# Kernel tuning notes

Measured on AMD Instinct MI355X. Metric: run time of the kernel, lower is better.

The kernel has to match this reference:

```python
import jax, jax.numpy as jnp
import numpy as np

HEADS = 12
D_MODEL = 768
D_K = D_MODEL // HEADS
BS, SEQ = 2, 4096


def setup_inputs() -> dict:
    key = jax.random.key(0)
    ks = jax.random.split(key, 12)
    s = 1.0 / np.sqrt(D_MODEL)
    return {
        "q": jax.random.normal(ks[0], (BS, SEQ, D_MODEL), jnp.float32),
        "k": jax.random.normal(ks[1], (BS, SEQ, D_MODEL), jnp.float32),
        "v": jax.random.normal(ks[2], (BS, SEQ, D_MODEL), jnp.float32),
        "Wq": jax.random.normal(ks[3], (D_MODEL, D_MODEL), jnp.float32) * s,
        "bq": jax.random.normal(ks[4], (D_MODEL,), jnp.float32) * s,
        "Wk": jax.random.normal(ks[5], (D_MODEL, D_MODEL), jnp.float32) * s,
        "bk": jax.random.normal(ks[6], (D_MODEL,), jnp.float32) * s,
        "Wv": jax.random.normal(ks[7], (D_MODEL, D_MODEL), jnp.float32) * s,
        "bv": jax.random.normal(ks[8], (D_MODEL,), jnp.float32) * s,
        "Wo": jax.random.normal(ks[9], (D_MODEL, D_MODEL), jnp.float32) * s,
        "bo": jax.random.normal(ks[10], (D_MODEL,), jnp.float32) * s,
        "mask": jnp.ones((BS, 1, SEQ), jnp.int32),
    }


def reference(q, k, v, Wq, bq, Wk, bk, Wv, bv, Wo, bo, mask):
    bs, sq, _ = q.shape
    # torch Linear: x @ W.T + b; then reshape to (bs, S, h, d_k) and transpose to (bs, h, S, d_k)
    def proj(x, W, b):
        y = x @ W.T + b
        return y.reshape(bs, -1, HEADS, D_K).transpose(0, 2, 1, 3)
    qh, kh, vh = proj(q, Wq, bq), proj(k, Wk, bk), proj(v, Wv, bv)
    scores = jnp.einsum("bhqd,bhkd->bhqk", qh, kh) / np.sqrt(D_K)
    # mask.unsqueeze(1): [bs,1,1,S_kv], masked_fill where mask == 0
    scores = jnp.where(mask[:, None, :, :] == 0, jnp.float32(-1e9), scores)
    attn = jax.nn.softmax(scores, axis=-1)  # dropout = identity (eval mode)
    ctx = jnp.einsum("bhqk,bhkd->bhqd", attn, vh)
    concat = ctx.transpose(0, 2, 1, 3).reshape(bs, sq, D_MODEL)
    return concat @ Wo.T + bo
```

## Files before the change

kernel.cpp:

```cpp
#include <hip/hip_runtime.h>
#include <hip/hip_bf16.h>

typedef __bf16 bf16x8 __attribute__((ext_vector_type(8)));
typedef float f32x4 __attribute__((ext_vector_type(4)));
typedef unsigned short u16;

#define HEADS 12
#define DK 64
#define DM 768
#define SEQL 4096
#define BSZ 2
#define MROWS (BSZ * SEQL)
#define WELEM (DM * DM)
#define NX 6291456
#define WTOT (4 * WELEM)
#define BTOT (4 * 768)

#define QSCALE 0.180336880434245f
#define EXP2F(x) __builtin_amdgcn_exp2f(x)

__device__ __forceinline__ float bf2f(u16 x) {
    unsigned int u = ((unsigned int)x) << 16;
    return __uint_as_float(u);
}
__device__ __forceinline__ u16 f2bf(float f) {
    unsigned int u = __float_as_uint(f);
    u += 0x7fff + ((u >> 16) & 1);
    return (u16)(u >> 16);
}
__device__ __forceinline__ unsigned int cvt_pk(float lo, float hi) {
#if __has_builtin(__builtin_amdgcn_cvt_pk_bf16_f32)
    auto r = __builtin_amdgcn_cvt_pk_bf16_f32(lo, hi);
    unsigned int u;
    __builtin_memcpy(&u, &r, 4);
    return u;
#else
    return (unsigned int)f2bf(lo) | ((unsigned int)f2bf(hi) << 16);
#endif
}

__global__ void detect_dtype(const u16* __restrict__ q, int* __restrict__ flag) {
    __shared__ int cnt;
    if (threadIdx.x == 0) cnt = 0;
    __syncthreads();
    int c = 0;
    for (int i = threadIdx.x; i < 16384; i += 256) {
        u16 x = q[i];
        if (((x >> 7) & 0xFF) == 0xFF) c++;
    }
    if (c) atomicAdd(&cnt, c);
    __syncthreads();
    if (threadIdx.x == 0) *flag = (cnt > 0) ? 1 : 0;
}

__global__ __launch_bounds__(256) void convert_x(
    const void* __restrict__ X0, const void* __restrict__ X1, const void* __restrict__ X2,
    u16* __restrict__ Xc, const int* __restrict__ flag) {
    const int f32m = *flag;
    int i8 = blockIdx.x * 256 + threadIdx.x;
    if (i8 >= 3 * NX / 8) return;
    int w = i8 / (NX / 8);
    int off8 = i8 - w * (NX / 8);
    const void* src = (w == 0) ? X0 : (w == 1) ? X1 : X2;
    u16* dst = Xc + (size_t)w * NX + (size_t)off8 * 8;
    if (f32m) {
        float4 f0 = ((const float4*)src)[off8 * 2];
        float4 f1 = ((const float4*)src)[off8 * 2 + 1];
        uint4 p = {cvt_pk(f0.x, f0.y), cvt_pk(f0.z, f0.w),
                   cvt_pk(f1.x, f1.y), cvt_pk(f1.z, f1.w)};
        *(uint4*)dst = p;
    } else {
        *(uint4*)dst = ((const uint4*)src)[off8];
    }
}

__global__ __launch_bounds__(256) void convert_wb(
    const void* __restrict__ W0, const void* __restrict__ W1,
    const void* __restrict__ W2, const void* __restrict__ W3,
    const void* __restrict__ B0, const void* __restrict__ B1,
    const void* __restrict__ B2, const void* __restrict__ B3,
    u16* __restrict__ Wc, u16* __restrict__ bc, const int* __restrict__ flag) {
    const int f32m = *flag;
    int i4 = blockIdx.x * 256 + threadIdx.x;
    const int n4 = (WTOT + BTOT) / 4;
    if (i4 >= n4) return;
    int base = i4 * 4;
    const void* src;
    u16* dst;
    int off;
    if (base < WTOT) {
        int w = base / WELEM;
        off = base - w * WELEM;
        src = (w == 0) ? W0 : (w == 1) ? W1 : (w == 2) ? W2 : W3;
        dst = Wc + w * WELEM + off;
    } else {
        int bi = base - WTOT;
        int w = bi / 768;
        off = bi - w * 768;
        src = (w == 0) ? B0 : (w == 1) ? B1 : (w == 2) ? B2 : B3;
        dst = bc + w * 768 + off;
    }
    if (f32m) {
        float4 f = *(const float4*)((const float*)src + off);
        uint2 p = {cvt_pk(f.x, f.y), cvt_pk(f.z, f.w)};
        *(uint2*)dst = p;
    } else {
        *(uint2*)dst = *(const uint2*)((const u16*)src + off);
    }
}

typedef __attribute__((address_space(1))) unsigned int glb_u32;
typedef __attribute__((address_space(3))) unsigned int lds_u32;

__device__ __forceinline__ void gld16(const u16* g, u16* l) {
    __builtin_amdgcn_global_load_lds((glb_u32*)g, (lds_u32*)l, 16, 0, 0);
}

template <int NCH>
__device__ __forceinline__ void stage_g(const u16* gbase, u16* lbase, int tid) {
#pragma unroll
    for (int it = 0; it < NCH / 256; ++it) {
        int c = it * 256 + tid;
        int row = c >> 2, p = c & 3;
        int gc = p ^ (row & 3);
        gld16(gbase + (size_t)row * DM + gc * 8, lbase + c * 8);
    }
}

__global__ __launch_bounds__(256) void gemm_qkv3(
    const u16* __restrict__ Xc, const u16* __restrict__ Wc, const u16* __restrict__ bc,
    u16* __restrict__ Yq, u16* __restrict__ Yk, u16* __restrict__ Yv) {
    __shared__ __align__(16) u16 As[2][128 * 32];
    __shared__ __align__(16) u16 Bs[2][128 * 32];

    const int by  = blockIdx.y;
    const int sel = by / 6;
    const int n0  = (by - sel * 6) * 128;
    const int m0  = blockIdx.x * 128;

    const u16* X  = Xc + (size_t)sel * NX;
    const u16* W  = Wc + (size_t)sel * WELEM;
    const u16* Bp = bc + sel * 768;
    u16* Y = sel == 0 ? Yq : (sel == 1 ? Yk : Yv);
    const float oscale = sel == 0 ? QSCALE : 1.0f;

    const int tid = threadIdx.x, lane = tid & 63, wave = tid >> 6;
    const int wr = (wave >> 1) * 64, wc2 = (wave & 1) * 64;
    const int l15 = lane & 15, quad = lane >> 4;
    const int ck = (quad ^ (l15 & 3)) * 8;

    f32x4 acc[4][4] = {};

    stage_g<512>(X + (size_t)m0 * DM, &As[0][0], tid);
    stage_g<512>(W + (size_t)n0 * DM, &Bs[0][0], tid);
    __syncthreads();

    for (int it = 0; it < 24; ++it) {
        const int cur = it & 1, nxt = cur ^ 1;
        if (it < 23) {
            stage_g<512>(X + (size_t)m0 * DM + (it + 1) * 32, &As[nxt][0], tid);
            stage_g<512>(W + (size_t)n0 * DM + (it + 1) * 32, &Bs[nxt][0], tid);
        }
        bf16x8 a[4], b[4];
#pragma unroll
        for (int i = 0; i < 4; ++i)
            a[i] = *(const bf16x8*)&As[cur][(wr + i * 16 + l15) * 32 + ck];
#pragma unroll
        for (int j = 0; j < 4; ++j)
            b[j] = *(const bf16x8*)&Bs[cur][(wc2 + j * 16 + l15) * 32 + ck];
#pragma unroll
        for (int i = 0; i < 4; ++i)
#pragma unroll
            for (int j = 0; j < 4; ++j)
                acc[i][j] = __builtin_amdgcn_mfma_f32_16x16x32_bf16(a[i], b[j], acc[i][j], 0, 0, 0);
        __syncthreads();
    }

#pragma unroll
    for (int j = 0; j < 4; ++j) {
        int o = n0 + wc2 + j * 16 + l15;
        float bv = bf2f(Bp[o]);
        int h = o >> 6, d = o & 63;
#pragma unroll
        for (int i = 0; i < 4; ++i) {
            int row0 = m0 + wr + i * 16 + quad * 4;
            int bb = row0 >> 12, s0 = row0 & (SEQL - 1);
            if (sel < 2) {
#pragma unroll
                for (int r = 0; r < 4; ++r)
                    Y[((bb * HEADS + h) << 18) + ((s0 + r) << 6) + d] =
                        f2bf((acc[i][j][r] + bv) * oscale);
            } else {
                uint2 p = {cvt_pk(acc[i][j][0] + bv, acc[i][j][1] + bv),
                           cvt_pk(acc[i][j][2] + bv, acc[i][j][3] + bv)};
                *(uint2*)&Y[((bb * HEADS + h) << 18) + (d << 12) + s0] = p;
            }
        }
    }
}

__global__ __launch_bounds__(256) void gemm_out3(const u16* __restrict__ X,
                                                 const u16* __restrict__ W,
                                                 const u16* __restrict__ Bp,
                                                 void* __restrict__ Y,
                                                 const int* __restrict__ flag) {
    __shared__ __align__(16) u16 As[2][64 * 32];
    __shared__ __align__(16) u16 Bs[2][128 * 32];

    const int f32mode = *flag;
    const int m0 = blockIdx.x * 64, n0 = blockIdx.y * 128;
    const int tid = threadIdx.x, lane = tid & 63, wave = tid >> 6;
    const int wr = (wave >> 1) * 32, wc2 = (wave & 1) * 64;
    const int l15 = lane & 15, quad = lane >> 4;
    const int ck = (quad ^ (l15 & 3)) * 8;

    f32x4 acc[2][4] = {};

    stage_g<256>(X + (size_t)m0 * DM, &As[0][0], tid);
    stage_g<512>(W + (size_t)n0 * DM, &Bs[0][0], tid);
    __syncthreads();

    for (int it = 0; it < 24; ++it) {
        const int cur = it & 1, nxt = cur ^ 1;
        if (it < 23) {
            stage_g<256>(X + (size_t)m0 * DM + (it + 1) * 32, &As[nxt][0], tid);
            stage_g<512>(W + (size_t)n0 * DM + (it + 1) * 32, &Bs[nxt][0], tid);
        }
        bf16x8 a[2], b[4];
#pragma unroll
        for (int i = 0; i < 2; ++i)
            a[i] = *(const bf16x8*)&As[cur][(wr + i * 16 + l15) * 32 + ck];
#pragma unroll
        for (int j = 0; j < 4; ++j)
            b[j] = *(const bf16x8*)&Bs[cur][(wc2 + j * 16 + l15) * 32 + ck];
#pragma unroll
        for (int i = 0; i < 2; ++i)
#pragma unroll
            for (int j = 0; j < 4; ++j)
                acc[i][j] = __builtin_amdgcn_mfma_f32_16x16x32_bf16(a[i], b[j], acc[i][j], 0, 0, 0);
        __syncthreads();
    }

#pragma unroll
    for (int j = 0; j < 4; ++j) {
        int o = n0 + wc2 + j * 16 + l15;
        float bv = bf2f(Bp[o]);
#pragma unroll
        for (int i = 0; i < 2; ++i)
#pragma unroll
            for (int r = 0; r < 4; ++r) {
                int row = m0 + wr + i * 16 + quad * 4 + r;
                float val = acc[i][j][r] + bv;
                if (f32mode) ((float*)Y)[(size_t)row * DM + o] = val;
                else         ((u16*)Y)[(size_t)row * DM + o] = f2bf(val);
            }
    }
}

__device__ __forceinline__ void stage8_bf16(u16* dst, const u16* src) {
    *(uint4*)dst = *(const uint4*)src;
}
__device__ __forceinline__ void stage16_bf16(u16* dst, const u16* src) {
    *(uint4*)dst = *(const uint4*)src;
    *(uint4*)(dst + 8) = *(const uint4*)(src + 8);
}
__device__ __forceinline__ void stage16_f32pk(u16* dst, const float* src) {
    float4 f0 = ((const float4*)src)[0];
    float4 f1 = ((const float4*)src)[1];
    float4 f2 = ((const float4*)src)[2];
    float4 f3 = ((const float4*)src)[3];
    uint4 lo = {cvt_pk(f0.x, f0.y), cvt_pk(f0.z, f0.w), cvt_pk(f1.x, f1.y), cvt_pk(f1.z, f1.w)};
    uint4 hi = {cvt_pk(f2.x, f2.y), cvt_pk(f2.z, f2.w), cvt_pk(f3.x, f3.y), cvt_pk(f3.z, f3.w)};
    *(uint4*)dst = lo;
    *(uint4*)(dst + 8) = hi;
}

__global__ __launch_bounds__(256) void gemm_qkv_fb(
    const void* __restrict__ Xq, const void* __restrict__ Xk, const void* __restrict__ Xv,
    const u16* __restrict__ Wc, const u16* __restrict__ bc,
    u16* __restrict__ Yq, u16* __restrict__ Yk, u16* __restrict__ Yv,
    const int* __restrict__ flag) {
    __shared__ __align__(16) u16 As[128][40];
    __shared__ __align__(16) u16 Bs[64][40];
    const int f32mode = *flag;
    const int by = blockIdx.y;
    const int sel = by / 12;
    const int n0 = (by - sel * 12) * 64;
    const int m0 = blockIdx.x * 128;
    const void* Xp = sel == 0 ? Xq : (sel == 1 ? Xk : Xv);
    const u16* Wp = Wc + sel * WELEM;
    const u16* Bp = bc + sel * 768;
    u16* Y = sel == 0 ? Yq : (sel == 1 ? Yk : Yv);
    const float oscale = sel == 0 ? QSCALE : 1.0f;
    const int tid = threadIdx.x, lane = tid & 63, wave = tid >> 6;
    const int wr = (wave >> 1) * 64, wc = (wave & 1) * 32;
    const int l15 = lane & 15, quad = lane >> 4;
    const int srA = tid >> 1, scA = (tid & 1) * 16;
    const int srB = tid >> 2, scB = (tid & 3) * 8;
    f32x4 acc[4][2] = {};
    const size_t xoff = (size_t)(m0 + srA) * DM + scA;
    const size_t woff = (size_t)(n0 + srB) * DM + scB;
    for (int kb = 0; kb < DM; kb += 32) {
        if (f32mode) stage16_f32pk(&As[srA][scA], (const float*)Xp + xoff + kb);
        else         stage16_bf16(&As[srA][scA], (const u16*)Xp + xoff + kb);
        stage8_bf16(&Bs[srB][scB], Wp + woff + kb);
        __syncthreads();
        bf16x8 a[4], b[2];
#pragma unroll
        for (int i = 0; i < 4; ++i) a[i] = *(const bf16x8*)&As[wr + i * 16 + l15][quad * 8];
#pragma unroll
        for (int j = 0; j < 2; ++j) b[j] = *(const bf16x8*)&Bs[wc + j * 16 + l15][quad * 8];
#pragma unroll
        for (int i = 0; i < 4; ++i)
#pragma unroll
            for (int j = 0; j < 2; ++j)
                acc[i][j] = __builtin_amdgcn_mfma_f32_16x16x32_bf16(a[i], b[j], acc[i][j], 0, 0, 0);
        __syncthreads();
    }
#pragma unroll
    for (int j = 0; j < 2; ++j) {
        int o = n0 + wc + j * 16 + l15;
        float bv = bf2f(Bp[o]);
#pragma unroll
        for (int i = 0; i < 4; ++i)
#pragma unroll
            for (int r = 0; r < 4; ++r) {
                int row = m0 + wr + i * 16 + quad * 4 + r;
                float val = (acc[i][j][r] + bv) * oscale;
                int bb = row >> 12, s = row & (SEQL - 1);
                int h = o >> 6, d = o & 63;
                if (sel < 2) Y[((bb * HEADS + h) << 18) + (s << 6) + d] = f2bf(val);
                else         Y[((bb * HEADS + h) << 18) + (d << 12) + s] = f2bf(val);
            }
    }
}

__global__ __launch_bounds__(256) void gemm_out_fb(const u16* __restrict__ X,
                                                   const u16* __restrict__ Wp,
                                                   const u16* __restrict__ Bp,
                                                   void* __restrict__ Y,
                                                   const int* __restrict__ flag) {
    __shared__ __align__(16) u16 As[128][40];
    __shared__ __align__(16) u16 Bs[64][40];
    const int f32mode = *flag;
    const int m0 = blockIdx.x * 128, n0 = blockIdx.y * 64;
    const int tid = threadIdx.x, lane = tid & 63, wave = tid >> 6;
    const int wr = (wave >> 1) * 64, wc = (wave & 1) * 32;
    const int l15 = lane & 15, quad = lane >> 4;
    const int srA = tid >> 1, scA = (tid & 1) * 16;
    const int srB = tid >> 2, scB = (tid & 3) * 8;
    f32x4 acc[4][2] = {};
    const size_t xoff = (size_t)(m0 + srA) * DM + scA;
    const size_t woff = (size_t)(n0 + srB) * DM + scB;
    for (int kb = 0; kb < DM; kb += 32) {
        stage16_bf16(&As[srA][scA], X + xoff + kb);
        stage8_bf16(&Bs[srB][scB], Wp + woff + kb);
        __syncthreads();
        bf16x8 a[4], b[2];
#pragma unroll
        for (int i = 0; i < 4; ++i) a[i] = *(const bf16x8*)&As[wr + i * 16 + l15][quad * 8];
#pragma unroll
        for (int j = 0; j < 2; ++j) b[j] = *(const bf16x8*)&Bs[wc + j * 16 + l15][quad * 8];
#pragma unroll
        for (int i = 0; i < 4; ++i)
#pragma unroll
            for (int j = 0; j < 2; ++j)
                acc[i][j] = __builtin_amdgcn_mfma_f32_16x16x32_bf16(a[i], b[j], acc[i][j], 0, 0, 0);
        __syncthreads();
    }
#pragma unroll
    for (int j = 0; j < 2; ++j) {
        int o = n0 + wc + j * 16 + l15;
        float bv = bf2f(Bp[o]);
#pragma unroll
        for (int i = 0; i < 4; ++i)
#pragma unroll
            for (int r = 0; r < 4; ++r) {
                int row = m0 + wr + i * 16 + quad * 4 + r;
                float val = acc[i][j][r] + bv;
                if (f32mode) ((float*)Y)[(size_t)row * DM + o] = val;
                else         ((u16*)Y)[(size_t)row * DM + o] = f2bf(val);
            }
    }
}

__device__ __forceinline__ void stage_tile(const u16* gbase, int rstride,
                                           u16* lbase, int tid) {
#pragma unroll
    for (int it = 0; it < 2; ++it) {
        int c = it * 256 + tid;
        int row = c >> 3, p = c & 7;
        int gc = p ^ (row & 7);
        gld16(gbase + (size_t)row * rstride + gc * 8, lbase + c * 8);
    }
}

__global__ __launch_bounds__(256, 3) void flash_attn(const u16* __restrict__ Q,
                                                     const u16* __restrict__ K,
                                                     const u16* __restrict__ Vt,
                                                     const int* __restrict__ mask,
                                                     u16* __restrict__ ctx) {
    __shared__ __align__(16) u16 Ks[2][64 * 64];
    __shared__ __align__(16) u16 Vs[2][64 * 64];
    __shared__ __align__(16) float Ms[2][64];
    __shared__ __align__(16) u16 Ps[4][32 * 72];

    const int tid  = threadIdx.x;
    const int lane = tid & 63;
    const int wave = tid >> 6;
    const int l15  = lane & 15;
    const int quad = lane >> 4;

    const int bh = blockIdx.y;
    const int b  = bh / HEADS;
    const int h  = bh - b * HEADS;
    const int qb = blockIdx.x * 128 + wave * 32;

    const u16* Qh = Q  + ((size_t)bh << 18);
    const u16* Kh = K  + ((size_t)bh << 18);
    const u16* Vh = Vt + ((size_t)bh << 18);
    const int* maskb = mask + b * SEQL;

    bf16x8 aq[2][2];
#pragma unroll
    for (int s = 0; s < 2; ++s)
#pragma unroll
        for (int c = 0; c < 2; ++c)
            aq[s][c] = *(const bf16x8*)&Qh[(size_t)(qb + s * 16 + l15) * DK + c * 32 + quad * 8];

    const int r7   = l15 & 7;
    const int ck0  = (quad ^ r7) * 8;
    const int ck1  = ((quad + 4) ^ r7) * 8;
    const int lrow = l15 * 64;

    float m_s[2] = {-3.0e38f, -3.0e38f}, l_s[2] = {0.f, 0.f};
    f32x4 o_acc[2][4] = {};

    int mreg = 0;
    if (tid < 64) mreg = maskb[tid];
    stage_tile(Kh, DK, &Ks[0][0], tid);
    stage_tile(Vh, SEQL, &Vs[0][0], tid);
    if (tid < 64) {
        Ms[0][tid] = (mreg == 0) ? -1.0e9f : 0.0f;
        mreg = maskb[64 + tid];
    }
    __syncthreads();

    for (int t = 0; t < 64; ++t) {
        const int cur = t & 1, nxt = cur ^ 1;
        if (t < 63) {
            const int kt = (t + 1) * 64;
            stage_tile(Kh + (size_t)kt * DK, DK, &Ks[nxt][0], tid);
            stage_tile(Vh + kt, SEQL, &Vs[nxt][0], tid);
            if (tid < 64) {
                Ms[nxt][tid] = (mreg == 0) ? -1.0e9f : 0.0f;
                if (t < 62) mreg = maskb[(t + 2) * 64 + tid];
            }
        }

        const u16* kb = &Ks[cur][0];
        const u16* vb = &Vs[cur][0];

        f32x4 s4[2][4];
#pragma unroll
        for (int nt = 0; nt < 4; ++nt) {
            bf16x8 ak0 = *(const bf16x8*)&kb[lrow + nt * 1024 + ck0];
            bf16x8 ak1 = *(const bf16x8*)&kb[lrow + nt * 1024 + ck1];
            f32x4 bias = *(const f32x4*)&Ms[cur][nt * 16 + quad * 4];
#pragma unroll
            for (int s = 0; s < 2; ++s) {
                f32x4 z = {};
                z = __builtin_amdgcn_mfma_f32_16x16x32_bf16(ak0, aq[s][0], z, 0, 0, 0);
                z = __builtin_amdgcn_mfma_f32_16x16x32_bf16(ak1, aq[s][1], z, 0, 0, 0);
#pragma unroll
                for (int r = 0; r < 4; ++r) s4[s][nt][r] = z[r] + bias[r];
            }
        }

        float newm[2], rs[2];
#pragma unroll
        for (int s = 0; s < 2; ++s) {
            float mx = -3.0e38f;
#pragma unroll
            for (int nt = 0; nt < 4; ++nt)
#pragma unroll
                for (int r = 0; r < 4; ++r) mx = fmaxf(mx, s4[s][nt][r]);
            mx = fmaxf(mx, __shfl_xor(mx, 16, 64));
            mx = fmaxf(mx, __shfl_xor(mx, 32, 64));
            newm[s] = fmaxf(m_s[s], mx);

            float r2 = 0.f;
#pragma unroll
            for (int nt = 0; nt < 4; ++nt)
#pragma unroll
                for (int r = 0; r < 4; ++r) {
                    float p = EXP2F(s4[s][nt][r] - newm[s]);
                    s4[s][nt][r] = p;
                    r2 += p;
                }
            r2 += __shfl_xor(r2, 16, 64);
            r2 += __shfl_xor(r2, 32, 64);
            rs[s] = r2;
        }

        if (!__all(newm[0] == m_s[0] && newm[1] == m_s[1])) {
#pragma unroll
            for (int s = 0; s < 2; ++s) {
                float alpha = EXP2F(m_s[s] - newm[s]);
                l_s[s] *= alpha;
#pragma unroll
                for (int dv = 0; dv < 4; ++dv)
#pragma unroll
                    for (int r = 0; r < 4; ++r) o_acc[s][dv][r] *= alpha;
                m_s[s] = newm[s];
            }
        }
        l_s[0] += rs[0];
        l_s[1] += rs[1];

#pragma unroll
        for (int s = 0; s < 2; ++s)
#pragma unroll
            for (int nt = 0; nt < 4; ++nt) {
                uint2 cv = {cvt_pk(s4[s][nt][0], s4[s][nt][1]),
                            cvt_pk(s4[s][nt][2], s4[s][nt][3])};
                *(uint2*)&Ps[wave][(s * 16 + l15) * 72 + nt * 16 + quad * 4] = cv;
            }
        asm volatile("" ::: "memory");

        bf16x8 bp[2][2];
#pragma unroll
        for (int s = 0; s < 2; ++s)
#pragma unroll
            for (int c = 0; c < 2; ++c)
                bp[s][c] = *(const bf16x8*)&Ps[wave][(s * 16 + l15) * 72 + c * 32 + quad * 8];

#pragma unroll
        for (int dv = 0; dv < 4; ++dv) {
            bf16x8 av0 = *(const bf16x8*)&vb[lrow + dv * 1024 + ck0];
            bf16x8 av1 = *(const bf16x8*)&vb[lrow + dv * 1024 + ck1];
#pragma unroll
            for (int s = 0; s < 2; ++s) {
                o_acc[s][dv] = __builtin_amdgcn_mfma_f32_16x16x32_bf16(av0, bp[s][0], o_acc[s][dv], 0, 0, 0);
                o_acc[s][dv] = __builtin_amdgcn_mfma_f32_16x16x32_bf16(av1, bp[s][1], o_acc[s][dv], 0, 0, 0);
            }
        }
        __syncthreads();
    }

#pragma unroll
    for (int s = 0; s < 2; ++s) {
        float inv = 1.0f / l_s[s];
#pragma unroll
        for (int dv = 0; dv < 4; ++dv) {
            uint2 cv = {cvt_pk(o_acc[s][dv][0] * inv, o_acc[s][dv][1] * inv),
                        cvt_pk(o_acc[s][dv][2] * inv, o_acc[s][dv][3] * inv)};
            *(uint2*)&Ps[wave][(s * 16 + l15) * 72 + dv * 16 + quad * 4] = cv;
        }
    }
    asm volatile("" ::: "memory");
    {
        int rowq = lane >> 2, dchunk = lane & 3;
#pragma unroll
        for (int s = 0; s < 2; ++s) {
            uint4 w0 = *(const uint4*)&Ps[wave][(s * 16 + rowq) * 72 + dchunk * 16];
            uint4 w1 = *(const uint4*)&Ps[wave][(s * 16 + rowq) * 72 + dchunk * 16 + 8];
            size_t orow = (size_t)(b * SEQL + qb + s * 16 + rowq) * DM + h * DK + dchunk * 16;
            *(uint4*)&ctx[orow] = w0;
            *(uint4*)&ctx[orow + 8] = w1;
        }
    }
}

extern "C" void kernel_launch(void* const* d_in, const int* in_sizes, int n_in,
                              void* d_out, int out_size, void* d_ws, size_t ws_size,
                              hipStream_t stream) {
    const void* q   = d_in[0];
    const void* k   = d_in[1];
    const void* v   = d_in[2];
    const void* Wq  = d_in[3];
    const void* bq  = d_in[4];
    const void* Wk  = d_in[5];
    const void* bk  = d_in[6];
    const void* Wv  = d_in[7];
    const void* bv  = d_in[8];
    const void* Wo  = d_in[9];
    const void* bo  = d_in[10];
    const int* mask = (const int*)d_in[11];

    const size_t NSH = (size_t)NX;
    u16* ws = (u16*)d_ws;

    const size_t need_full = (6 * NSH + WTOT + BTOT) * sizeof(u16) + 64;
    const size_t need_fb   = (4 * NSH + WTOT + BTOT) * sizeof(u16) + 64;

    if (ws_size >= need_full) {
        u16* Qh  = ws;
        u16* Kh  = ws + NSH;
        u16* Vth = ws + 2 * NSH;
        u16* Xc  = ws + 3 * NSH;
        u16* ctx = Xc;
        u16* Wc  = ws + 6 * NSH;
        u16* bc  = Wc + WTOT;
        int* dflag = (int*)(bc + BTOT);

        detect_dtype<<<1, 256, 0, stream>>>((const u16*)q, dflag);
        convert_x<<<(3 * NX / 8 + 255) / 256, 256, 0, stream>>>(q, k, v, Xc, dflag);
        convert_wb<<<((WTOT + BTOT) / 4 + 255) / 256, 256, 0, stream>>>(
            Wq, Wk, Wv, Wo, bq, bk, bv, bo, Wc, bc, dflag);

        gemm_qkv3<<<dim3(MROWS / 128, 18), 256, 0, stream>>>(Xc, Wc, bc, Qh, Kh, Vth);
        flash_attn<<<dim3(SEQL / 128, BSZ * HEADS), 256, 0, stream>>>(Qh, Kh, Vth, mask, ctx);
        gemm_out3<<<dim3(MROWS / 64, 6), 256, 0, stream>>>(
            ctx, Wc + 3 * (size_t)WELEM, bc + 3 * 768, d_out, dflag);
    } else if (ws_size >= need_fb) {
        u16* Qh  = ws;
        u16* Kh  = ws + NSH;
        u16* Vth = ws + 2 * NSH;
        u16* ctx = ws + 3 * NSH;
        u16* Wc  = ws + 4 * NSH;
        u16* bc  = Wc + WTOT;
        int* dflag = (int*)(bc + BTOT);

        detect_dtype<<<1, 256, 0, stream>>>((const u16*)q, dflag);
        convert_wb<<<((WTOT + BTOT) / 4 + 255) / 256, 256, 0, stream>>>(
            Wq, Wk, Wv, Wo, bq, bk, bv, bo, Wc, bc, dflag);
        gemm_qkv_fb<<<dim3(MROWS / 128, 36), 256, 0, stream>>>(
            q, k, v, Wc, bc, Qh, Kh, Vth, dflag);
        flash_attn<<<dim3(SEQL / 128, BSZ * HEADS), 256, 0, stream>>>(Qh, Kh, Vth, mask, ctx);
        gemm_out_fb<<<dim3(MROWS / 128, 12), 256, 0, stream>>>(
            ctx, Wc + 3 * (size_t)WELEM, bc + 3 * 768, d_out, dflag);
    }
}
```

Before: 416.0 us.

## Restructure flash attention to 8 waves of 16 query rows with register-resident P

Flash attention now launches 512 threads per block, with each of 8 waves owning 16 query rows instead of 4 waves owning 32. The softmax probabilities stay in registers and feed a 16x16x16 bf16 MFMA directly, which removes the per-wave LDS round trip for P. V fragments are read from the swizzled tile in 4-element pieces. The mask bias add is skipped when a tile has no masked keys, and K/V tile staging is spread across twice as many threads. In exchange, each K/V tile is reused by fewer rows per wave, the smaller MFMA shape may have lower throughput, and the extra waves raise occupancy and scheduling pressure.

```diff
diff --git a/kernel.cpp b/kernel.cpp
--- a/kernel.cpp
+++ b/kernel.cpp
@@ -2,6 +2,8 @@
 #include <hip/hip_bf16.h>
 
 typedef __bf16 bf16x8 __attribute__((ext_vector_type(8)));
+typedef __bf16 bf16x4 __attribute__((ext_vector_type(4)));
+typedef short s16x4 __attribute__((ext_vector_type(4)));
 typedef float f32x4 __attribute__((ext_vector_type(4)));
 typedef unsigned short u16;
 
@@ -36,6 +38,21 @@
     return u;
 #else
     return (unsigned int)f2bf(lo) | ((unsigned int)f2bf(hi) << 16);
+#endif
+}
+
+__device__ __forceinline__ f32x4 mfma16(bf16x4 a, bf16x4 b, f32x4 c) {
+#if __has_builtin(__builtin_amdgcn_mfma_f32_16x16x16_bf16)
+    return __builtin_amdgcn_mfma_f32_16x16x16_bf16(a, b, c, 0, 0, 0);
+#elif __has_builtin(__builtin_amdgcn_mfma_f32_16x16x16bf16_1k)
+    s16x4 ai, bi;
+    __builtin_memcpy(&ai, &a, 8);
+    __builtin_memcpy(&bi, &b, 8);
+    return __builtin_amdgcn_mfma_f32_16x16x16bf16_1k(ai, bi, c, 0, 0, 0);
+#else
+    f32x4 d = c;
+    asm("v_mfma_f32_16x16x16_bf16 %0, %1, %2, %0" : "+v"(d) : "v"(a), "v"(b));
+    return d;
 #endif
 }
 
@@ -384,26 +401,21 @@
     }
 }
 
-__device__ __forceinline__ void stage_tile(const u16* gbase, int rstride,
-                                           u16* lbase, int tid) {
-#pragma unroll
-    for (int it = 0; it < 2; ++it) {
-        int c = it * 256 + tid;
-        int row = c >> 3, p = c & 7;
-        int gc = p ^ (row & 7);
-        gld16(gbase + (size_t)row * rstride + gc * 8, lbase + c * 8);
-    }
-}
-
-__global__ __launch_bounds__(256, 3) void flash_attn(const u16* __restrict__ Q,
+__device__ __forceinline__ void stage_tile8(const u16* gbase, int rstride,
+                                            u16* lbase, int tid) {
+    int row = tid >> 3, p = tid & 7;
+    int gc = p ^ (row & 7);
+    gld16(gbase + (size_t)row * rstride + gc * 8, lbase + tid * 8);
+}
+
+__global__ __launch_bounds__(512, 6) void flash_attn(const u16* __restrict__ Q,
                                                      const u16* __restrict__ K,
                                                      const u16* __restrict__ Vt,
                                                      const int* __restrict__ mask,
                                                      u16* __restrict__ ctx) {
-    __shared__ __align__(16) u16 Ks[2][64 * 64];
-    __shared__ __align__(16) u16 Vs[2][64 * 64];
+    __shared__ __align__(16) u16 KVs[2][2][64 * 64];
     __shared__ __align__(16) float Ms[2][64];
-    __shared__ __align__(16) u16 Ps[4][32 * 72];
+    __shared__ int Mf[2];
 
     const int tid  = threadIdx.x;
     const int lane = tid & 63;
@@ -414,34 +426,36 @@
     const int bh = blockIdx.y;
     const int b  = bh / HEADS;
     const int h  = bh - b * HEADS;
-    const int qb = blockIdx.x * 128 + wave * 32;
+    const int qb = blockIdx.x * 128 + wave * 16;
 
     const u16* Qh = Q  + ((size_t)bh << 18);
     const u16* Kh = K  + ((size_t)bh << 18);
     const u16* Vh = Vt + ((size_t)bh << 18);
     const int* maskb = mask + b * SEQL;
 
-    bf16x8 aq[2][2];
-#pragma unroll
-    for (int s = 0; s < 2; ++s)
-#pragma unroll
-        for (int c = 0; c < 2; ++c)
-            aq[s][c] = *(const bf16x8*)&Qh[(size_t)(qb + s * 16 + l15) * DK + c * 32 + quad * 8];
+    bf16x8 aq[2];
+#pragma unroll
+    for (int c = 0; c < 2; ++c)
+        aq[c] = *(const bf16x8*)&Qh[(size_t)(qb + l15) * DK + c * 32 + quad * 8];
 
     const int r7   = l15 & 7;
     const int ck0  = (quad ^ r7) * 8;
     const int ck1  = ((quad + 4) ^ r7) * 8;
     const int lrow = l15 * 64;
-
-    float m_s[2] = {-3.0e38f, -3.0e38f}, l_s[2] = {0.f, 0.f};
-    f32x4 o_acc[2][4] = {};
+    const int vq   = quad >> 1;
+    const int voff = (quad & 1) * 4;
+
+    float m_s = -3.0e38f, l_s = 0.f;
+    f32x4 o_acc[4] = {};
 
     int mreg = 0;
     if (tid < 64) mreg = maskb[tid];
-    stage_tile(Kh, DK, &Ks[0][0], tid);
-    stage_tile(Vh, SEQL, &Vs[0][0], tid);
+    stage_tile8(Kh, DK, &KVs[0][0][0], tid);
+    stage_tile8(Vh, SEQL, &KVs[0][1][0], tid);
     if (tid < 64) {
+        int anym = __any(mreg == 0);
         Ms[0][tid] = (mreg == 0) ? -1.0e9f : 0.0f;
+        if (tid == 0) Mf[0] = anym;
         mreg = maskb[64 + tid];
     }
     __syncthreads();
@@ -450,125 +464,111 @@
         const int cur = t & 1, nxt = cur ^ 1;
         if (t < 63) {
             const int kt = (t + 1) * 64;
-            stage_tile(Kh + (size_t)kt * DK, DK, &Ks[nxt][0], tid);
-            stage_tile(Vh + kt, SEQL, &Vs[nxt][0], tid);
+            stage_tile8(Kh + (size_t)kt * DK, DK, &KVs[nxt][0][0], tid);
+            stage_tile8(Vh + kt, SEQL, &KVs[nxt][1][0], tid);
             if (tid < 64) {
+                int anym = __any(mreg == 0);
                 Ms[nxt][tid] = (mreg == 0) ? -1.0e9f : 0.0f;
+                if (tid == 0) Mf[nxt] = anym;
                 if (t < 62) mreg = maskb[(t + 2) * 64 + tid];
             }
         }
 
-        const u16* kb = &Ks[cur][0];
-        const u16* vb = &Vs[cur][0];
-
-        f32x4 s4[2][4];
+        const u16* kb = &KVs[cur][0][0];
+        const u16* vb = &KVs[cur][1][0];
+        const int usebias = Mf[cur];
+
+        f32x4 s4[4];
 #pragma unroll
         for (int nt = 0; nt < 4; ++nt) {
             bf16x8 ak0 = *(const bf16x8*)&kb[lrow + nt * 1024 + ck0];
             bf16x8 ak1 = *(const bf16x8*)&kb[lrow + nt * 1024 + ck1];
-            f32x4 bias = *(const f32x4*)&Ms[cur][nt * 16 + quad * 4];
-#pragma unroll
-            for (int s = 0; s < 2; ++s) {
-                f32x4 z = {};
-                z = __builtin_amdgcn_mfma_f32_16x16x32_bf16(ak0, aq[s][0], z, 0, 0, 0);
-                z = __builtin_amdgcn_mfma_f32_16x16x32_bf16(ak1, aq[s][1], z, 0, 0, 0);
-#pragma unroll
-                for (int r = 0; r < 4; ++r) s4[s][nt][r] = z[r] + bias[r];
+            f32x4 z = {};
+            z = __builtin_amdgcn_mfma_f32_16x16x32_bf16(ak0, aq[0], z, 0, 0, 0);
+            z = __builtin_amdgcn_mfma_f32_16x16x32_bf16(ak1, aq[1], z, 0, 0, 0);
+            s4[nt] = z;
+        }
+        if (usebias) {
+#pragma unroll
+            for (int nt = 0; nt < 4; ++nt) {
+                f32x4 bias = *(const f32x4*)&Ms[cur][nt * 16 + quad * 4];
+#pragma unroll
+                for (int r = 0; r < 4; ++r) s4[nt][r] += bias[r];
             }
         }
 
-        float newm[2], rs[2];
-#pragma unroll
-        for (int s = 0; s < 2; ++s) {
-            float mx = -3.0e38f;
+        float t0 = fmaxf(fmaxf(s4[0][0], s4[0][1]), fmaxf(s4[0][2], s4[0][3]));
+        float t1 = fmaxf(fmaxf(s4[1][0], s4[1][1]), fmaxf(s4[1][2], s4[1][3]));
+        float t2 = fmaxf(fmaxf(s4[2][0], s4[2][1]), fmaxf(s4[2][2], s4[2][3]));
+        float t3 = fmaxf(fmaxf(s4[3][0], s4[3][1]), fmaxf(s4[3][2], s4[3][3]));
+        float mx = fmaxf(fmaxf(t0, t1), fmaxf(t2, t3));
+        mx = fmaxf(mx, __shfl_xor(mx, 16, 64));
+        mx = fmaxf(mx, __shfl_xor(mx, 32, 64));
+        float newm = fmaxf(m_s, mx);
+
+        f32x4 psum = {};
+#pragma unroll
+        for (int nt = 0; nt < 4; ++nt)
+#pragma unroll
+            for (int r = 0; r < 4; ++r) {
+                float p = EXP2F(s4[nt][r] - newm);
+                s4[nt][r] = p;
+                psum[nt] += p;
+            }
+        float r2 = (psum[0] + psum[1]) + (psum[2] + psum[3]);
+        r2 += __shfl_xor(r2, 16, 64);
+        r2 += __shfl_xor(r2, 32, 64);
+
+        if (!__all(newm == m_s)) {
+            float alpha = EXP2F(m_s - newm);
+            l_s *= alpha;
+#pragma unroll
+            for (int dv = 0; dv < 4; ++dv)
+#pragma unroll
+                for (int r = 0; r < 4; ++r) o_acc[dv][r] *= alpha;
+            m_s = newm;
+        }
+        l_s += r2;
+
+        bf16x4 pp[4];
+#pragma unroll
+        for (int nt = 0; nt < 4; ++nt) {
+            uint2 cv = {cvt_pk(s4[nt][0], s4[nt][1]), cvt_pk(s4[nt][2], s4[nt][3])};
+            __builtin_memcpy(&pp[nt], &cv, 8);
+        }
+
+#pragma unroll
+        for (int dv = 0; dv < 4; ++dv) {
+            bf16x4 av[4];
 #pragma unroll
             for (int nt = 0; nt < 4; ++nt)
-#pragma unroll
-                for (int r = 0; r < 4; ++r) mx = fmaxf(mx, s4[s][nt][r]);
-            mx = fmaxf(mx, __shfl_xor(mx, 16, 64));
-            mx = fmaxf(mx, __shfl_xor(mx, 32, 64));
-            newm[s] = fmaxf(m_s[s], mx);
-
-            float r2 = 0.f;
+                av[nt] = *(const bf16x4*)&vb[(dv * 16 + l15) * 64 +
+                                            (((nt << 1) | vq) ^ r7) * 8 + voff];
 #pragma unroll
             for (int nt = 0; nt < 4; ++nt)
-#pragma unroll
-                for (int r = 0; r < 4; ++r) {
-                    float p = EXP2F(s4[s][nt][r] - newm[s]);
-                    s4[s][nt][r] = p;
-                    r2 += p;
-                }
-            r2 += __shfl_xor(r2, 16, 64);
-            r2 += __shfl_xor(r2, 32, 64);
-            rs[s] = r2;
-        }
-
-        if (!__all(newm[0] == m_s[0] && newm[1] == m_s[1])) {
-#pragma unroll
-            for (int s = 0; s < 2; ++s) {
-                float alpha = EXP2F(m_s[s] - newm[s]);
-                l_s[s] *= alpha;
-#pragma unroll
-                for (int dv = 0; dv < 4; ++dv)
-#pragma unroll
-                    for (int r = 0; r < 4; ++r) o_acc[s][dv][r] *= alpha;
-                m_s[s] = newm[s];
-            }
-        }
-        l_s[0] += rs[0];
-        l_s[1] += rs[1];
-
-#pragma unroll
-        for (int s = 0; s < 2; ++s)
-#pragma unroll
-            for (int nt = 0; nt < 4; ++nt) {
-                uint2 cv = {cvt_pk(s4[s][nt][0], s4[s][nt][1]),
-                            cvt_pk(s4[s][nt][2], s4[s][nt][3])};
-                *(uint2*)&Ps[wave][(s * 16 + l15) * 72 + nt * 16 + quad * 4] = cv;
-            }
-        asm volatile("" ::: "memory");
-
-        bf16x8 bp[2][2];
-#pragma unroll
-        for (int s = 0; s < 2; ++s)
-#pragma unroll
-            for (int c = 0; c < 2; ++c)
-                bp[s][c] = *(const bf16x8*)&Ps[wave][(s * 16 + l15) * 72 + c * 32 + quad * 8];
-
+                o_acc[dv] = mfma16(av[nt], pp[nt], o_acc[dv]);
+        }
+        __syncthreads();
+    }
+
+    u16* eb = &KVs[0][0][0] + wave * 1152;
+    {
+        float inv = 1.0f / l_s;
 #pragma unroll
         for (int dv = 0; dv < 4; ++dv) {
-            bf16x8 av0 = *(const bf16x8*)&vb[lrow + dv * 1024 + ck0];
-            bf16x8 av1 = *(const bf16x8*)&vb[lrow + dv * 1024 + ck1];
-#pragma unroll
-            for (int s = 0; s < 2; ++s) {
-                o_acc[s][dv] = __builtin_amdgcn_mfma_f32_16x16x32_bf16(av0, bp[s][0], o_acc[s][dv], 0, 0, 0);
-                o_acc[s][dv] = __builtin_amdgcn_mfma_f32_16x16x32_bf16(av1, bp[s][1], o_acc[s][dv], 0, 0, 0);
-            }
-        }
-        __syncthreads();
-    }
-
-#pragma unroll
-    for (int s = 0; s < 2; ++s) {
-        float inv = 1.0f / l_s[s];
-#pragma unroll
-        for (int dv = 0; dv < 4; ++dv) {
-            uint2 cv = {cvt_pk(o_acc[s][dv][0] * inv, o_acc[s][dv][1] * inv),
-                        cvt_pk(o_acc[s][dv][2] * inv, o_acc[s][dv][3] * inv)};
-            *(uint2*)&Ps[wave][(s * 16 + l15) * 72 + dv * 16 + quad * 4] = cv;
+            uint2 cv = {cvt_pk(o_acc[dv][0] * inv, o_acc[dv][1] * inv),
+                        cvt_pk(o_acc[dv][2] * inv, o_acc[dv][3] * inv)};
+            *(uint2*)&eb[l15 * 72 + dv * 16 + quad * 4] = cv;
         }
     }
     asm volatile("" ::: "memory");
     {
         int rowq = lane >> 2, dchunk = lane & 3;
-#pragma unroll
-        for (int s = 0; s < 2; ++s) {
-            uint4 w0 = *(const uint4*)&Ps[wave][(s * 16 + rowq) * 72 + dchunk * 16];
-            uint4 w1 = *(const uint4*)&Ps[wave][(s * 16 + rowq) * 72 + dchunk * 16 + 8];
-            size_t orow = (size_t)(b * SEQL + qb + s * 16 + rowq) * DM + h * DK + dchunk * 16;
-            *(uint4*)&ctx[orow] = w0;
-            *(uint4*)&ctx[orow + 8] = w1;
-        }
+        uint4 w0 = *(const uint4*)&eb[rowq * 72 + dchunk * 16];
+        uint4 w1 = *(const uint4*)&eb[rowq * 72 + dchunk * 16 + 8];
+        size_t orow = (size_t)(b * SEQL + qb + rowq) * DM + h * DK + dchunk * 16;
+        *(uint4*)&ctx[orow] = w0;
+        *(uint4*)&ctx[orow + 8] = w1;
     }
 }
 
@@ -610,7 +610,7 @@
             Wq, Wk, Wv, Wo, bq, bk, bv, bo, Wc, bc, dflag);
 
         gemm_qkv3<<<dim3(MROWS / 128, 18), 256, 0, stream>>>(Xc, Wc, bc, Qh, Kh, Vth);
-        flash_attn<<<dim3(SEQL / 128, BSZ * HEADS), 256, 0, stream>>>(Qh, Kh, Vth, mask, ctx);
+        flash_attn<<<dim3(SEQL / 128, BSZ * HEADS), 512, 0, stream>>>(Qh, Kh, Vth, mask, ctx);
         gemm_out3<<<dim3(MROWS / 64, 6), 256, 0, stream>>>(
             ctx, Wc + 3 * (size_t)WELEM, bc + 3 * 768, d_out, dflag);
     } else if (ws_size >= need_fb) {
@@ -627,7 +627,7 @@
             Wq, Wk, Wv, Wo, bq, bk, bv, bo, Wc, bc, dflag);
         gemm_qkv_fb<<<dim3(MROWS / 128, 36), 256, 0, stream>>>(
             q, k, v, Wc, bc, Qh, Kh, Vth, dflag);
-        flash_attn<<<dim3(SEQL / 128, BSZ * HEADS), 256, 0, stream>>>(Qh, Kh, Vth, mask, ctx);
+        flash_attn<<<dim3(SEQL / 128, BSZ * HEADS), 512, 0, stream>>>(Qh, Kh, Vth, mask, ctx);
         gemm_out_fb<<<dim3(MROWS / 128, 12), 256, 0, stream>>>(
             ctx, Wc + 3 * (size_t)WELEM, bc + 3 * 768, d_out, dflag);
     }
```

Result: slower. 472.3 us (+13.5%).

## Feed softmax probabilities to PV MFMA from registers, skip mask bias when unmasked

Applied to the files above, without the earlier changes.

The PV product now uses 16x16x16 MFMAs whose B operand layout matches the S accumulator layout. The bf16 probabilities go straight from registers into the MFMA, removing the per-wave LDS write and read-back of P. The mask bias add is skipped for tiles where a per-tile flag shows no masked keys. The change also adds tree-shaped max and sum reductions and raises wave priority around the MFMA block. The P buffer is gone, which frees LDS for occupancy, and the epilogue reuses the K/V buffers; the cost is twice as many smaller MFMA instructions and narrower V loads.

```diff
diff --git a/kernel.cpp b/kernel.cpp
--- a/kernel.cpp
+++ b/kernel.cpp
@@ -2,6 +2,8 @@
 #include <hip/hip_bf16.h>
 
 typedef __bf16 bf16x8 __attribute__((ext_vector_type(8)));
+typedef __bf16 bf16x4 __attribute__((ext_vector_type(4)));
+typedef short s16x4 __attribute__((ext_vector_type(4)));
 typedef float f32x4 __attribute__((ext_vector_type(4)));
 typedef unsigned short u16;
 
@@ -36,6 +38,21 @@
     return u;
 #else
     return (unsigned int)f2bf(lo) | ((unsigned int)f2bf(hi) << 16);
+#endif
+}
+
+__device__ __forceinline__ f32x4 mfma16(bf16x4 a, bf16x4 b, f32x4 c) {
+#if __has_builtin(__builtin_amdgcn_mfma_f32_16x16x16_bf16)
+    return __builtin_amdgcn_mfma_f32_16x16x16_bf16(a, b, c, 0, 0, 0);
+#elif __has_builtin(__builtin_amdgcn_mfma_f32_16x16x16bf16_1k)
+    s16x4 ai, bi;
+    __builtin_memcpy(&ai, &a, 8);
+    __builtin_memcpy(&bi, &b, 8);
+    return __builtin_amdgcn_mfma_f32_16x16x16bf16_1k(ai, bi, c, 0, 0, 0);
+#else
+    f32x4 d = c;
+    asm("v_mfma_f32_16x16x16_bf16 %0, %1, %2, %0" : "+v"(d) : "v"(a), "v"(b));
+    return d;
 #endif
 }
 
@@ -400,10 +417,9 @@
                                                      const u16* __restrict__ Vt,
                                                      const int* __restrict__ mask,
                                                      u16* __restrict__ ctx) {
-    __shared__ __align__(16) u16 Ks[2][64 * 64];
-    __shared__ __align__(16) u16 Vs[2][64 * 64];
+    __shared__ __align__(16) u16 KVs[2][2][64 * 64];
     __shared__ __align__(16) float Ms[2][64];
-    __shared__ __align__(16) u16 Ps[4][32 * 72];
+    __shared__ int Mf[2];
 
     const int tid  = threadIdx.x;
     const int lane = tid & 63;
@@ -432,16 +448,20 @@
     const int ck0  = (quad ^ r7) * 8;
     const int ck1  = ((quad + 4) ^ r7) * 8;
     const int lrow = l15 * 64;
+    const int vq   = quad >> 1;
+    const int voff = (quad & 1) * 4;
 
     float m_s[2] = {-3.0e38f, -3.0e38f}, l_s[2] = {0.f, 0.f};
     f32x4 o_acc[2][4] = {};
 
     int mreg = 0;
     if (tid < 64) mreg = maskb[tid];
-    stage_tile(Kh, DK, &Ks[0][0], tid);
-    stage_tile(Vh, SEQL, &Vs[0][0], tid);
+    stage_tile(Kh, DK, &KVs[0][0][0], tid);
+    stage_tile(Vh, SEQL, &KVs[0][1][0], tid);
     if (tid < 64) {
+        int anym = __any(mreg == 0);
         Ms[0][tid] = (mreg == 0) ? -1.0e9f : 0.0f;
+        if (tid == 0) Mf[0] = anym;
         mreg = maskb[64 + tid];
     }
     __syncthreads();
@@ -450,54 +470,66 @@
         const int cur = t & 1, nxt = cur ^ 1;
         if (t < 63) {
             const int kt = (t + 1) * 64;
-            stage_tile(Kh + (size_t)kt * DK, DK, &Ks[nxt][0], tid);
-            stage_tile(Vh + kt, SEQL, &Vs[nxt][0], tid);
+            stage_tile(Kh + (size_t)kt * DK, DK, &KVs[nxt][0][0], tid);
+            stage_tile(Vh + kt, SEQL, &KVs[nxt][1][0], tid);
             if (tid < 64) {
+                int anym = __any(mreg == 0);
                 Ms[nxt][tid] = (mreg == 0) ? -1.0e9f : 0.0f;
+                if (tid == 0) Mf[nxt] = anym;
                 if (t < 62) mreg = maskb[(t + 2) * 64 + tid];
             }
         }
 
-        const u16* kb = &Ks[cur][0];
-        const u16* vb = &Vs[cur][0];
+        const u16* kb = &KVs[cur][0][0];
+        const u16* vb = &KVs[cur][1][0];
+        const int usebias = Mf[cur];
 
         f32x4 s4[2][4];
 #pragma unroll
         for (int nt = 0; nt < 4; ++nt) {
             bf16x8 ak0 = *(const bf16x8*)&kb[lrow + nt * 1024 + ck0];
             bf16x8 ak1 = *(const bf16x8*)&kb[lrow + nt * 1024 + ck1];
-            f32x4 bias = *(const f32x4*)&Ms[cur][nt * 16 + quad * 4];
 #pragma unroll
             for (int s = 0; s < 2; ++s) {
                 f32x4 z = {};
                 z = __builtin_amdgcn_mfma_f32_16x16x32_bf16(ak0, aq[s][0], z, 0, 0, 0);
                 z = __builtin_amdgcn_mfma_f32_16x16x32_bf16(ak1, aq[s][1], z, 0, 0, 0);
-#pragma unroll
-                for (int r = 0; r < 4; ++r) s4[s][nt][r] = z[r] + bias[r];
+                s4[s][nt] = z;
+            }
+        }
+        if (usebias) {
+#pragma unroll
+            for (int nt = 0; nt < 4; ++nt) {
+                f32x4 bias = *(const f32x4*)&Ms[cur][nt * 16 + quad * 4];
+#pragma unroll
+                for (int s = 0; s < 2; ++s)
+#pragma unroll
+                    for (int r = 0; r < 4; ++r) s4[s][nt][r] += bias[r];
             }
         }
 
         float newm[2], rs[2];
 #pragma unroll
         for (int s = 0; s < 2; ++s) {
-            float mx = -3.0e38f;
-#pragma unroll
-            for (int nt = 0; nt < 4; ++nt)
-#pragma unroll
-                for (int r = 0; r < 4; ++r) mx = fmaxf(mx, s4[s][nt][r]);
+            float t0 = fmaxf(fmaxf(s4[s][0][0], s4[s][0][1]), fmaxf(s4[s][0][2], s4[s][0][3]));
+            float t1 = fmaxf(fmaxf(s4[s][1][0], s4[s][1][1]), fmaxf(s4[s][1][2], s4[s][1][3]));
+            float t2 = fmaxf(fmaxf(s4[s][2][0], s4[s][2][1]), fmaxf(s4[s][2][2], s4[s][2][3]));
+            float t3 = fmaxf(fmaxf(s4[s][3][0], s4[s][3][1]), fmaxf(s4[s][3][2], s4[s][3][3]));
+            float mx = fmaxf(fmaxf(t0, t1), fmaxf(t2, t3));
             mx = fmaxf(mx, __shfl_xor(mx, 16, 64));
             mx = fmaxf(mx, __shfl_xor(mx, 32, 64));
             newm[s] = fmaxf(m_s[s], mx);
 
-            float r2 = 0.f;
+            f32x4 psum = {};
 #pragma unroll
             for (int nt = 0; nt < 4; ++nt)
 #pragma unroll
                 for (int r = 0; r < 4; ++r) {
                     float p = EXP2F(s4[s][nt][r] - newm[s]);
                     s4[s][nt][r] = p;
-                    r2 += p;
+                    psum[nt] += p;
                 }
+            float r2 = (psum[0] + psum[1]) + (psum[2] + psum[3]);
             r2 += __shfl_xor(r2, 16, 64);
             r2 += __shfl_xor(r2, 32, 64);
             rs[s] = r2;
@@ -518,36 +550,37 @@
         l_s[0] += rs[0];
         l_s[1] += rs[1];
 
+        bf16x4 pp[2][4];
 #pragma unroll
         for (int s = 0; s < 2; ++s)
 #pragma unroll
             for (int nt = 0; nt < 4; ++nt) {
                 uint2 cv = {cvt_pk(s4[s][nt][0], s4[s][nt][1]),
                             cvt_pk(s4[s][nt][2], s4[s][nt][3])};
-                *(uint2*)&Ps[wave][(s * 16 + l15) * 72 + nt * 16 + quad * 4] = cv;
-            }
-        asm volatile("" ::: "memory");
-
-        bf16x8 bp[2][2];
-#pragma unroll
-        for (int s = 0; s < 2; ++s)
-#pragma unroll
-            for (int c = 0; c < 2; ++c)
-                bp[s][c] = *(const bf16x8*)&Ps[wave][(s * 16 + l15) * 72 + c * 32 + quad * 8];
-
-#pragma unroll
-        for (int dv = 0; dv < 4; ++dv) {
-            bf16x8 av0 = *(const bf16x8*)&vb[lrow + dv * 1024 + ck0];
-            bf16x8 av1 = *(const bf16x8*)&vb[lrow + dv * 1024 + ck1];
-#pragma unroll
-            for (int s = 0; s < 2; ++s) {
-                o_acc[s][dv] = __builtin_amdgcn_mfma_f32_16x16x32_bf16(av0, bp[s][0], o_acc[s][dv], 0, 0, 0);
-                o_acc[s][dv] = __builtin_amdgcn_mfma_f32_16x16x32_bf16(av1, bp[s][1], o_acc[s][dv], 0, 0, 0);
-            }
-        }
+                __builtin_memcpy(&pp[s][nt], &cv, 8);
+            }
+
+        bf16x4 av[4][4];
+#pragma unroll
+        for (int dv = 0; dv < 4; ++dv)
+#pragma unroll
+            for (int nt = 0; nt < 4; ++nt)
+                av[dv][nt] = *(const bf16x4*)&vb[(dv * 16 + l15) * 64 +
+                                                (((nt << 1) | vq) ^ r7) * 8 + voff];
+
+        __builtin_amdgcn_s_setprio(1);
+#pragma unroll
+        for (int nt = 0; nt < 4; ++nt)
+#pragma unroll
+            for (int dv = 0; dv < 4; ++dv)
+#pragma unroll
+                for (int s = 0; s < 2; ++s)
+                    o_acc[s][dv] = mfma16(av[dv][nt], pp[s][nt], o_acc[s][dv]);
+        __builtin_amdgcn_s_setprio(0);
         __syncthreads();
     }
 
+    u16* eb = &KVs[0][0][0] + wave * 2304;
 #pragma unroll
     for (int s = 0; s < 2; ++s) {
         float inv = 1.0f / l_s[s];
@@ -555,7 +588,7 @@
         for (int dv = 0; dv < 4; ++dv) {
             uint2 cv = {cvt_pk(o_acc[s][dv][0] * inv, o_acc[s][dv][1] * inv),
                         cvt_pk(o_acc[s][dv][2] * inv, o_acc[s][dv][3] * inv)};
-            *(uint2*)&Ps[wave][(s * 16 + l15) * 72 + dv * 16 + quad * 4] = cv;
+            *(uint2*)&eb[(s * 16 + l15) * 72 + dv * 16 + quad * 4] = cv;
         }
     }
     asm volatile("" ::: "memory");
@@ -563,8 +596,8 @@
         int rowq = lane >> 2, dchunk = lane & 3;
 #pragma unroll
         for (int s = 0; s < 2; ++s) {
-            uint4 w0 = *(const uint4*)&Ps[wave][(s * 16 + rowq) * 72 + dchunk * 16];
-            uint4 w1 = *(const uint4*)&Ps[wave][(s * 16 + rowq) * 72 + dchunk * 16 + 8];
+            uint4 w0 = *(const uint4*)&eb[(s * 16 + rowq) * 72 + dchunk * 16];
+            uint4 w1 = *(const uint4*)&eb[(s * 16 + rowq) * 72 + dchunk * 16 + 8];
             size_t orow = (size_t)(b * SEQL + qb + s * 16 + rowq) * DM + h * DK + dchunk * 16;
             *(uint4*)&ctx[orow] = w0;
             *(uint4*)&ctx[orow + 8] = w1;
```

Result: faster. 403.1 us (-3.1%).
